# Kernel optimization log

Measured on AMD Instinct MI355X. Metric: run time of the kernel, lower is better.

## Reference

```python
import jax, jax.numpy as jnp
import numpy as np

T, B, DIN, H, DM, HYP, L = 128, 512, 512, 512, 256, 256, 100
STDV = 1.0 / np.sqrt(H)  # reset_parameters: uniform(-1/sqrt(hidden), 1/sqrt(hidden)) for ALL params
EPS = 1e-5


def setup_inputs() -> dict:
    key = jax.random.key(0)
    it = iter(jax.random.split(key, 32))
    U = lambda s: jax.random.uniform(next(it), s, jnp.float32, -STDV, STDV)
    x = jax.random.normal(next(it), (T, B, DIN), jnp.float32)
    meta = jax.random.normal(next(it), (B, L, DM), jnp.float32)
    inp = jax.random.randint(next(it), (B, L), 0, 5)
    return dict(
        x=x, meta=meta, inp=inp,
        # AttnModel (query from x, keys from meta)
        Wq=U((HYP, DIN)), bq=U((HYP,)), Wk=U((HYP, DM)), bk=U((HYP,)),
        # MergeLayer fc1 (fc2 is unused in MergeLayer.forward)
        Wm=U((HYP, DIN + DM + H)), bm=U((HYP,)),
        # hypernetwork projections z_h/z_x/z_b
        Wzh=U((4 * HYP, HYP)), bzh=U((4 * HYP,)),
        Wzx=U((4 * HYP, HYP)), bzx=U((4 * HYP,)),
        Wzb=U((4 * HYP, HYP)),
        # per-gate d_h/d_x/d_b maps (stacked over the 4 gates)
        Wdh=U((4, H, HYP)), Wdx=U((4, H, HYP)), Wdb=U((4, H, HYP)), bdb=U((4, H)),
        # main LSTM weights
        w_h=U((4, H, H)), w_x=U((4, H, DIN)),
        # per-gate LayerNorm affine
        ln_g=U((4, H)), ln_b=U((4, H)),
    )


def reference(x, meta, inp, Wq, bq, Wk, bk, Wm, bm, Wzh, bzh, Wzx, bzx, Wzb,
              Wdh, Wdx, Wdb, bdb, w_h, w_x, ln_g, ln_b):
    # --- AttnModel: attention-pool meta per timestep, meta_fea = [x, attended] ---
    q = jnp.einsum('tbi,hi->tbh', x, Wq) + bq                       # [T,B,HYP]
    k = jnp.einsum('blm,hm->blh', meta, Wk) + bk                    # [B,L,HYP]
    scores = jnp.einsum('tbh,blh->tbl', q, k) / jnp.sqrt(jnp.float32(HYP))
    scores = jnp.where((inp == 0)[None], -1e9, scores)              # pad mask
    attn = jax.nn.softmax(scores, axis=-1)
    attended = jnp.einsum('tbl,blm->tbm', attn, meta)               # [T,B,DM]
    meta_fea = jnp.concatenate([x, attended], axis=-1)              # [T,B,DIN+DM]

    def step(carry, xs):
        h, c = carry
        x_t, mf_t = xs
        # MergeLayer: relu(fc1(cat([meta_fea_t, h])))
        merged = jax.nn.relu(jnp.concatenate([mf_t, h], -1) @ Wm.T + bm)  # [B,HYP]
        zh = (merged @ Wzh.T + bzh).reshape(B, 4, HYP)
        zx = (merged @ Wzx.T + bzx).reshape(B, 4, HYP)
        zb = (merged @ Wzb.T).reshape(B, 4, HYP)
        d_h = jnp.einsum('bkz,khz->bkh', zh, Wdh)
        d_x = jnp.einsum('bkz,khz->bkh', zx, Wdx)
        d_b = jnp.einsum('bkz,khz->bkh', zb, Wdb) + bdb
        wh = jnp.einsum('khj,bj->bkh', w_h, h)
        wx = jnp.einsum('khj,bj->bkh', w_x, x_t)
        y = d_h * wh + d_x * wx + d_b                               # [B,4,H]
        mu = y.mean(-1, keepdims=True)
        var = ((y - mu) ** 2).mean(-1, keepdims=True)
        y = (y - mu) / jnp.sqrt(var + EPS) * ln_g + ln_b
        i, f, g, o = y[:, 0], y[:, 1], y[:, 2], y[:, 3]
        c_n = jax.nn.sigmoid(f) * c + jax.nn.sigmoid(i) * jnp.tanh(g)
        h_n = jax.nn.sigmoid(o) * jnp.tanh(c_n)
        return (h_n, c_n), h_n

    h0 = jnp.zeros((B, H), x.dtype)
    c0 = jnp.zeros((B, H), x.dtype)
    (hT, cT), out = jax.lax.scan(step, (h0, c0), (x, meta_fea))
    h_hat = jnp.zeros((1, B, HYP), x.dtype)  # hyper-state unused in this cell
    return out, hT[None], cT[None], h_hat, h_hat
```

## Files before the change

### kernel.cpp

```cpp
#include <hip/hip_runtime.h>
#include <hip/hip_bf16.h>

typedef unsigned short ushort_t;
typedef __attribute__((ext_vector_type(8))) short bf16x8;
typedef __attribute__((ext_vector_type(4))) float f32x4;

#define T_DIM 128
#define B_DIM 512
#define DIN 512
#define H_DIM 512
#define DM 256
#define HYP 256
#define L_DIM 100

__device__ __forceinline__ float bf2f(ushort_t u) {
    return __uint_as_float(((unsigned)u) << 16);
}
__device__ __forceinline__ ushort_t f2bf(float f) {
    unsigned u = __float_as_uint(f);
    unsigned r = (u + 0x7fffu + ((u >> 16) & 1u)) >> 16;
    return (ushort_t)r;
}
__device__ __forceinline__ float sigmoidf_(float x) {
    return 1.0f / (1.0f + __expf(-x));
}
__device__ __forceinline__ float fixf(float v) {
    if (!(v == v)) return 0.f;
    return fminf(fmaxf(v, -65504.f), 65504.f);
}

__global__ __launch_bounds__(256) void detect_kernel(const ushort_t* x, int nscan, int* flag) {
    __shared__ int found;
    if (threadIdx.x == 0) found = 0;
    __syncthreads();
    int f = 0;
    for (int i = threadIdx.x; i < nscan; i += 256) {
        unsigned u = x[i];
        if ((u & 0x7F80u) == 0x7F80u) f = 1;
    }
    if (f) atomicOr(&found, 1);
    __syncthreads();
    if (threadIdx.x == 0) *flag = found;
}

struct IngestP {
    const void* src[21];
    ushort_t* dst[21];
    int n[21];
    long total;
    const int* flag;
};

__global__ __launch_bounds__(256) void ingest_all(IngestP p) {
    int f = *p.flag;
    long idx0 = (long)blockIdx.x * 256 + threadIdx.x;
    long stride = (long)gridDim.x * 256;
    for (long idx = idx0; idx < p.total; idx += stride) {
        long r = idx;
#pragma unroll 1
        for (int t = 0; t < 21; t++) {
            if (r < p.n[t]) {
                p.dst[t][r] = f ? f2bf(((const float*)p.src[t])[r])
                               : ((const ushort_t*)p.src[t])[r];
                break;
            }
            r -= p.n[t];
        }
    }
}

__global__ __launch_bounds__(256) void zero_hhat(void* outbase, const int* flagp) {
    long i = 34078720 + (long)blockIdx.x * 256 + threadIdx.x;
    if (*flagp) ((float*)outbase)[i] = 0.f;
    else        ((ushort_t*)outbase)[i] = 0;
}

struct GP {
    const ushort_t* A1; const ushort_t* A2;
    const ushort_t* W1; const ushort_t* W2;
    long lda1, lda2, ldw1, ldw2;
    int K1, wc1, wc2, Nsplit, K, mode;
    const ushort_t* bias; ushort_t* outb; long ldo;
    const ushort_t* pre; ushort_t* merged; float* wh;
    float* outf; const float* fbias;
};

__global__ __launch_bounds__(256) void gemm_bt(GP g) {
    __shared__ __attribute__((aligned(16))) ushort_t As[128 * 40];
    __shared__ __attribute__((aligned(16))) ushort_t Bs[128 * 40];
    int tid  = threadIdx.x;
    int lane = tid & 63, wave = tid >> 6;
    int wm = (wave & 1) * 64, wn = (wave >> 1) * 64;
    int ml = lane & 15, quad = lane >> 4;
    long rowA0 = (long)blockIdx.x * 128;
    long rowW0 = (long)blockIdx.y * 128;
    int arow = tid >> 2, acol = (tid & 3) * 8;

    f32x4 acc[4][4];
#pragma unroll
    for (int i = 0; i < 4; i++)
#pragma unroll
        for (int j = 0; j < 4; j++) acc[i][j] = (f32x4){0.f, 0.f, 0.f, 0.f};

    for (int k0 = 0; k0 < g.K; k0 += 32) {
        uint4 av[2], wv[2];
#pragma unroll
        for (int s = 0; s < 2; s++) {
            int r = arow + s * 64;
            int k = k0 + acol;
            const ushort_t* asrc = (k < g.K1)
                ? g.A1 + (rowA0 + r) * g.lda1 + k
                : g.A2 + (rowA0 + r) * g.lda2 + (k - g.K1);
            av[s] = *(const uint4*)asrc;
            long n = rowW0 + r;
            const ushort_t* wsrc = (n < g.Nsplit)
                ? g.W1 + n * g.ldw1 + g.wc1 + k
                : g.W2 + (n - g.Nsplit) * g.ldw2 + g.wc2 + k;
            wv[s] = *(const uint4*)wsrc;
        }
        __syncthreads();
#pragma unroll
        for (int s = 0; s < 2; s++) {
            *(uint4*)&As[(arow + s * 64) * 40 + acol] = av[s];
            *(uint4*)&Bs[(arow + s * 64) * 40 + acol] = wv[s];
        }
        __syncthreads();
        bf16x8 af[4], bfm[4];
#pragma unroll
        for (int i = 0; i < 4; i++)
            af[i] = *(const bf16x8*)&As[(wm + i * 16 + ml) * 40 + quad * 8];
#pragma unroll
        for (int j = 0; j < 4; j++)
            bfm[j] = *(const bf16x8*)&Bs[(wn + j * 16 + ml) * 40 + quad * 8];
#pragma unroll
        for (int i = 0; i < 4; i++)
#pragma unroll
            for (int j = 0; j < 4; j++)
                acc[i][j] = __builtin_amdgcn_mfma_f32_16x16x32_bf16(af[i], bfm[j], acc[i][j], 0, 0, 0);
    }

#pragma unroll
    for (int i = 0; i < 4; i++) {
#pragma unroll
        for (int j = 0; j < 4; j++) {
            long rb = rowA0 + wm + i * 16 + quad * 4;
            long cn = rowW0 + wn + j * 16 + ml;
#pragma unroll
            for (int r = 0; r < 4; r++) {
                float v = acc[i][j][r];
                long rr = rb + r;
                if (g.mode == 0) {
                    if (g.bias) v += bf2f(g.bias[cn]);
                    g.outb[rr * g.ldo + cn] = f2bf(v);
                } else if (g.mode == 1) {
                    if (cn < 256) {
                        v += bf2f(g.pre[rr * 256 + cn]);
                        v = v > 0.f ? v : 0.f;
                        g.merged[rr * 256 + cn] = f2bf(v);
                    } else {
                        g.wh[rr * 2048 + (cn - 256)] = v;
                    }
                } else {
                    g.outf[rr * g.ldo + cn] = v + g.fbias[cn];
                }
            }
        }
    }
}

__global__ __launch_bounds__(256) void attn_kernel(const ushort_t* q, const ushort_t* kmat,
                                                   const ushort_t* meta, const int* inp,
                                                   ushort_t* att) {
    int b = blockIdx.x;
    __shared__ __attribute__((aligned(16))) ushort_t klds[L_DIM * 264];
    __shared__ float qlds[256];
    __shared__ float sc[L_DIM];
    __shared__ int msk[L_DIM];
    __shared__ float inv_s;
    int tid = threadIdx.x;

    for (int idx = tid; idx < L_DIM * 32; idx += 256) {
        int r = idx >> 5, c8 = (idx & 31) * 8;
        *(uint4*)&klds[r * 264 + c8] = *(const uint4*)&kmat[((long)b * L_DIM + r) * 256 + c8];
    }
    if (tid < L_DIM) msk[tid] = inp[b * L_DIM + tid];

    for (int t = 0; t < T_DIM; t++) {
        __syncthreads();
        qlds[tid] = bf2f(q[((long)t * B_DIM + b) * 256 + tid]);
        __syncthreads();
        if (tid < 2 * L_DIM) {
            int l = tid >> 1, half = tid & 1;
            const ushort_t* kr = &klds[l * 264 + half * 128];
            const float* qp = &qlds[half * 128];
            float s = 0.f;
            for (int j = 0; j < 128; j++) s += qp[j] * bf2f(kr[j]);
            s += __shfl_xor(s, 1);
            if (half == 0) sc[l] = (msk[l] == 0) ? -1000000000.0f : s * 0.0625f;
        }
        __syncthreads();
        if (tid < 64) {
            float s1 = sc[tid];
            float s2 = (tid + 64 < L_DIM) ? sc[tid + 64] : -1e30f;
            float mx = fmaxf(s1, s2);
            for (int o = 1; o < 64; o <<= 1) mx = fmaxf(mx, __shfl_xor(mx, o));
            float e1 = __expf(s1 - mx);
            float e2 = (tid + 64 < L_DIM) ? __expf(s2 - mx) : 0.f;
            float tot = e1 + e2;
            for (int o = 1; o < 64; o <<= 1) tot += __shfl_xor(tot, o);
            sc[tid] = e1;
            if (tid + 64 < L_DIM) sc[tid + 64] = e2;
            if (tid == 0) inv_s = 1.0f / tot;
        }
        __syncthreads();
        float a = 0.f;
        const ushort_t* mb = &meta[(long)b * L_DIM * 256 + tid];
        for (int l = 0; l < L_DIM; l++) a += sc[l] * bf2f(mb[(long)l * 256]);
        a *= inv_s;
        att[((long)t * B_DIM + b) * 256 + tid] = f2bf(a);
    }
}

__global__ __launch_bounds__(256) void call_precompute(const ushort_t* Wdh, const ushort_t* Wdx,
                                                       const ushort_t* Wdb, const ushort_t* Wzh,
                                                       const ushort_t* Wzx, const ushort_t* Wzb,
                                                       ushort_t* Call) {
    int bk = blockIdx.x;
    int kind = bk >> 2, kk = bk & 3;
    int h0 = blockIdx.y * 64;
    int m0 = blockIdx.z * 64;
    const ushort_t* Wd = (kind == 0) ? Wdh : ((kind == 1) ? Wdx : Wdb);
    const ushort_t* Wz = (kind == 0) ? Wzh : ((kind == 1) ? Wzx : Wzb);
    __shared__ __attribute__((aligned(16))) ushort_t dt[64 * 72];
    __shared__ __attribute__((aligned(16))) ushort_t zt[64 * 72];
    int tid = threadIdx.x;
    int ty = tid >> 4, tx = tid & 15;
    float acc[4][4] = {};
    for (int z0 = 0; z0 < 256; z0 += 64) {
        __syncthreads();
        for (int idx = tid; idx < 512; idx += 256) {
            int r = idx >> 3, c8 = (idx & 7) * 8;
            *(uint4*)&dt[r * 72 + c8] = *(const uint4*)&Wd[((long)(kk * 512 + h0 + r)) * 256 + z0 + c8];
            *(uint4*)&zt[r * 72 + c8] = *(const uint4*)&Wz[((long)(kk * 256 + z0 + r)) * 256 + m0 + c8];
        }
        __syncthreads();
        for (int z = 0; z < 64; z++) {
            float a[4], bb[4];
#pragma unroll
            for (int i = 0; i < 4; i++) a[i] = bf2f(dt[(ty * 4 + i) * 72 + z]);
#pragma unroll
            for (int j = 0; j < 4; j++) bb[j] = bf2f(zt[z * 72 + tx * 4 + j]);
#pragma unroll
            for (int i = 0; i < 4; i++)
#pragma unroll
                for (int j = 0; j < 4; j++) acc[i][j] += a[i] * bb[j];
        }
    }
#pragma unroll
    for (int i = 0; i < 4; i++)
#pragma unroll
        for (int j = 0; j < 4; j++)
            Call[((long)(kind * 2048 + kk * 512 + h0 + ty * 4 + i)) * 256 + m0 + tx * 4 + j] = f2bf(acc[i][j]);
}

__global__ __launch_bounds__(256) void dbias_kernel(const ushort_t* Wdh, const ushort_t* Wdx,
                                                    const ushort_t* bzh, const ushort_t* bzx,
                                                    const ushort_t* bdb, float* dbias) {
    int n = blockIdx.x * 256 + threadIdx.x;
    int kind = n >> 11, kk = (n >> 9) & 3, h = n & 511;
    float s = 0.f;
    if (kind == 2) {
        s = bf2f(bdb[kk * 512 + h]);
    } else {
        const ushort_t* Wd = (kind == 0) ? Wdh : Wdx;
        const ushort_t* bz = (kind == 0) ? bzh : bzx;
        for (int z = 0; z < 256; z++)
            s += bf2f(Wd[((long)(kk * 512 + h)) * 256 + z]) * bf2f(bz[kk * 256 + z]);
    }
    dbias[n] = s;
}

__global__ __launch_bounds__(256) void step_elem(const float* dall, const float* wh,
                                                 const ushort_t* wx, float* c, ushort_t* hbf,
                                                 const ushort_t* ln_g, const ushort_t* ln_b,
                                                 void* outbase, long off_t, int last,
                                                 const int* flagp) {
    int b = blockIdx.x, tid = threadIdx.x;
    int w = tid >> 6, lane = tid & 63;
    __shared__ float yln[4 * 512];
    const float* db = dall + (long)b * 6144;
    const float* whb = wh + (long)b * 2048;
    const ushort_t* wxb = wx + (long)b * 2048;
    float y[8];
    float sum = 0.f, ss = 0.f;
#pragma unroll
    for (int j = 0; j < 8; j++) {
        int h = lane + j * 64;
        int n = w * 512 + h;
        float v = db[n] * whb[n] + db[2048 + n] * bf2f(wxb[n]) + db[4096 + n];
        v = fixf(v);
        y[j] = v;
        sum += v;
        ss += v * v;
    }
    for (int o = 1; o < 64; o <<= 1) {
        sum += __shfl_xor(sum, o);
        ss += __shfl_xor(ss, o);
    }
    float mu = sum * (1.f / 512.f);
    float var = ss * (1.f / 512.f) - mu * mu;
    float rstd = rsqrtf(fmaxf(var, 0.f) + 1e-5f);
#pragma unroll
    for (int j = 0; j < 8; j++) {
        int h = lane + j * 64;
        float g = bf2f(ln_g[w * 512 + h]);
        float bb = bf2f(ln_b[w * 512 + h]);
        yln[w * 512 + h] = (y[j] - mu) * rstd * g + bb;
    }
    __syncthreads();
    int f = *flagp;
#pragma unroll
    for (int s = 0; s < 2; s++) {
        int h = tid + s * 256;
        float iv = yln[h], fv = yln[512 + h], gv = yln[1024 + h], ov = yln[1536 + h];
        long ci = (long)b * 512 + h;
        float cold = c[ci];
        float cn = sigmoidf_(fv) * cold + sigmoidf_(iv) * tanhf(gv);
        float hn = sigmoidf_(ov) * tanhf(cn);
        c[ci] = cn;
        hbf[ci] = f2bf(hn);
        if (f) {
            float* of = (float*)outbase;
            of[off_t + ci] = hn;
            if (last) { of[33554432 + ci] = hn; of[33816576 + ci] = cn; }
        } else {
            ushort_t* ob = (ushort_t*)outbase;
            ob[off_t + ci] = f2bf(hn);
            if (last) { ob[33554432 + ci] = f2bf(hn); ob[33816576 + ci] = f2bf(cn); }
        }
    }
}

extern "C" void kernel_launch(void* const* d_in, const int* in_sizes, int n_in,
                              void* d_out, int out_size, void* d_ws, size_t ws_size,
                              hipStream_t stream) {
    const int* inp = (const int*)d_in[2];

    size_t off = 0;
    char* wsb = (char*)d_ws;
    auto alloc = [&](size_t bytes) -> void* {
        off = (off + 255) & ~(size_t)255;
        void* p = wsb + off;
        off += bytes;
        return p;
    };

    int* flagp = (int*)alloc(256);

    static const int fidx[21] = {0,1,3,4,5,6,7,8,9,10,11,12,13,14,15,16,17,18,19,20,21};
    IngestP ip{};
    long total = 0;
    ushort_t* canon[21];
    for (int t = 0; t < 21; t++) {
        int src_i = fidx[t];
        int n = in_sizes[src_i];
        canon[t] = (ushort_t*)alloc((size_t)n * 2);
        ip.src[t] = d_in[src_i];
        ip.dst[t] = canon[t];
        ip.n[t] = n;
        total += n;
    }
    ip.total = total;
    ip.flag = flagp;

    const ushort_t* x    = canon[0];
    const ushort_t* meta = canon[1];
    const ushort_t* Wq   = canon[2];
    const ushort_t* bq   = canon[3];
    const ushort_t* Wk   = canon[4];
    const ushort_t* bk   = canon[5];
    const ushort_t* Wm   = canon[6];
    const ushort_t* bm   = canon[7];
    const ushort_t* Wzh  = canon[8];
    const ushort_t* bzh  = canon[9];
    const ushort_t* Wzx  = canon[10];
    const ushort_t* bzx  = canon[11];
    const ushort_t* Wzb  = canon[12];
    const ushort_t* Wdh  = canon[13];
    const ushort_t* Wdx  = canon[14];
    const ushort_t* Wdb  = canon[15];
    const ushort_t* bdb  = canon[16];
    const ushort_t* w_h  = canon[17];
    const ushort_t* w_x  = canon[18];
    const ushort_t* ln_g = canon[19];
    const ushort_t* ln_b = canon[20];

    ushort_t* qb    = (ushort_t*)alloc(33554432);
    ushort_t* kmb   = (ushort_t*)alloc(26214400);
    ushort_t* attb  = (ushort_t*)alloc(33554432);
    ushort_t* preb  = (ushort_t*)alloc(33554432);
    ushort_t* callb = (ushort_t*)alloc(3145728);
    float*    dbias = (float*)alloc(24576);
    ushort_t* hbf   = (ushort_t*)alloc(524288);
    float*    cf    = (float*)alloc(1048576);
    ushort_t* mgd   = (ushort_t*)alloc(262144);
    float*    whf   = (float*)alloc(4194304);
    float*    dall  = (float*)alloc(12582912);
    size_t base_end = (off + 255) & ~(size_t)255;
    bool full = (base_end + 268435456ull) <= ws_size;
    ushort_t* wxb = (ushort_t*)alloc(full ? 268435456ull : 2097152ull);

    detect_kernel<<<dim3(1), 256, 0, stream>>>((const ushort_t*)d_in[0], 262144, flagp);
    ingest_all<<<dim3(2048), 256, 0, stream>>>(ip);
    zero_hhat<<<dim3(1024), 256, 0, stream>>>(d_out, flagp);
    hipMemsetAsync(hbf, 0, 524288, stream);
    hipMemsetAsync(cf, 0, 1048576, stream);

    const int BIG = 1 << 30;

    {
        GP g{};
        g.A1 = meta; g.lda1 = 256; g.K1 = BIG; g.A2 = meta; g.lda2 = 256;
        g.W1 = Wk; g.ldw1 = 256; g.wc1 = 0; g.Nsplit = BIG; g.W2 = Wk; g.ldw2 = 256; g.wc2 = 0;
        g.K = 256; g.mode = 0; g.bias = bk; g.outb = kmb; g.ldo = 256;
        gemm_bt<<<dim3(400, 2), 256, 0, stream>>>(g);
    }
    {
        GP g{};
        g.A1 = x; g.lda1 = 512; g.K1 = BIG; g.A2 = x; g.lda2 = 512;
        g.W1 = Wq; g.ldw1 = 512; g.wc1 = 0; g.Nsplit = BIG; g.W2 = Wq; g.ldw2 = 512; g.wc2 = 0;
        g.K = 512; g.mode = 0; g.bias = bq; g.outb = qb; g.ldo = 256;
        gemm_bt<<<dim3(512, 2), 256, 0, stream>>>(g);
    }
    attn_kernel<<<dim3(512), 256, 0, stream>>>(qb, kmb, meta, inp, attb);
    {
        GP g{};
        g.A1 = x; g.lda1 = 512; g.K1 = 512; g.A2 = attb; g.lda2 = 256;
        g.W1 = Wm; g.ldw1 = 1280; g.wc1 = 0; g.Nsplit = BIG; g.W2 = Wm; g.ldw2 = 1280; g.wc2 = 0;
        g.K = 768; g.mode = 0; g.bias = bm; g.outb = preb; g.ldo = 256;
        gemm_bt<<<dim3(512, 2), 256, 0, stream>>>(g);
    }
    if (full) {
        GP g{};
        g.A1 = x; g.lda1 = 512; g.K1 = BIG; g.A2 = x; g.lda2 = 512;
        g.W1 = w_x; g.ldw1 = 512; g.wc1 = 0; g.Nsplit = BIG; g.W2 = w_x; g.ldw2 = 512; g.wc2 = 0;
        g.K = 512; g.mode = 0; g.bias = nullptr; g.outb = wxb; g.ldo = 2048;
        gemm_bt<<<dim3(512, 16), 256, 0, stream>>>(g);
    }
    call_precompute<<<dim3(12, 8, 4), 256, 0, stream>>>(Wdh, Wdx, Wdb, Wzh, Wzx, Wzb, callb);
    dbias_kernel<<<dim3(24), 256, 0, stream>>>(Wdh, Wdx, bzh, bzx, bdb, dbias);

    for (int t = 0; t < T_DIM; t++) {
        if (!full) {
            GP g{};
            g.A1 = x + (long)t * B_DIM * DIN; g.lda1 = 512; g.K1 = BIG; g.A2 = g.A1; g.lda2 = 512;
            g.W1 = w_x; g.ldw1 = 512; g.wc1 = 0; g.Nsplit = BIG; g.W2 = w_x; g.ldw2 = 512; g.wc2 = 0;
            g.K = 512; g.mode = 0; g.bias = nullptr; g.outb = wxb; g.ldo = 2048;
            gemm_bt<<<dim3(4, 16), 256, 0, stream>>>(g);
        }
        {
            GP g{};
            g.A1 = hbf; g.lda1 = 512; g.K1 = BIG; g.A2 = hbf; g.lda2 = 512;
            g.W1 = Wm; g.ldw1 = 1280; g.wc1 = 768; g.Nsplit = 256;
            g.W2 = w_h; g.ldw2 = 512; g.wc2 = 0;
            g.K = 512; g.mode = 1;
            g.pre = preb + (long)t * B_DIM * 256; g.merged = mgd; g.wh = whf;
            gemm_bt<<<dim3(4, 18), 256, 0, stream>>>(g);
        }
        {
            GP g{};
            g.A1 = mgd; g.lda1 = 256; g.K1 = BIG; g.A2 = mgd; g.lda2 = 256;
            g.W1 = callb; g.ldw1 = 256; g.wc1 = 0; g.Nsplit = BIG; g.W2 = callb; g.ldw2 = 256; g.wc2 = 0;
            g.K = 256; g.mode = 2; g.outf = dall; g.ldo = 6144; g.fbias = dbias;
            gemm_bt<<<dim3(4, 48), 256, 0, stream>>>(g);
        }
        const ushort_t* wxt = full ? (wxb + (long)t * B_DIM * 2048) : wxb;
        step_elem<<<dim3(512), 256, 0, stream>>>(dall, whf, wxt, cf, hbf, ln_g, ln_b,
                                                 d_out, (long)t * B_DIM * H_DIM,
                                                 (t == T_DIM - 1) ? 1 : 0, flagp);
    }
}
```

Measured before the change: 13.00 ms.

## Replace per-timestep kernel launches with a persistent cooperative kernel using grid sync

The recurrent scan previously launched three or four kernels per timestep, 128 timesteps in all. A single cooperative kernel with 256 blocks now loops over timesteps, distributes the GEMM tiles and per-batch elementwise work across blocks, and separates the dependent phases with grid.sync. This is meant to remove kernel launch and drain overhead on the serial critical path. The cost is grid-wide barriers and fixed tile assignment, so some blocks sit idle (e.g. only 72 tiles in the first phase), and it relies on all blocks being co-resident.

```diff
diff --git a/kernel.cpp b/kernel.cpp
--- a/kernel.cpp
+++ b/kernel.cpp
@@ -1,5 +1,8 @@
 #include <hip/hip_runtime.h>
 #include <hip/hip_bf16.h>
+#include <hip/hip_cooperative_groups.h>
+
+namespace cg = cooperative_groups;
 
 typedef unsigned short ushort_t;
 typedef __attribute__((ext_vector_type(8))) short bf16x8;
@@ -12,6 +15,7 @@
 #define DM 256
 #define HYP 256
 #define L_DIM 100
+#define GRID_P 256
 
 __device__ __forceinline__ float bf2f(ushort_t u) {
     return __uint_as_float(((unsigned)u) << 16);
@@ -85,15 +89,12 @@
     float* outf; const float* fbias;
 };
 
-__global__ __launch_bounds__(256) void gemm_bt(GP g) {
-    __shared__ __attribute__((aligned(16))) ushort_t As[128 * 40];
-    __shared__ __attribute__((aligned(16))) ushort_t Bs[128 * 40];
+__device__ __forceinline__ void gemm_tile(const GP& g, long rowA0, long rowW0,
+                                          ushort_t* As, ushort_t* Bs) {
     int tid  = threadIdx.x;
     int lane = tid & 63, wave = tid >> 6;
     int wm = (wave & 1) * 64, wn = (wave >> 1) * 64;
     int ml = lane & 15, quad = lane >> 4;
-    long rowA0 = (long)blockIdx.x * 128;
-    long rowW0 = (long)blockIdx.y * 128;
     int arow = tid >> 2, acol = (tid & 3) * 8;
 
     f32x4 acc[4][4];
@@ -168,6 +169,12 @@
     }
 }
 
+__global__ __launch_bounds__(256) void gemm_bt(GP g) {
+    __shared__ __attribute__((aligned(16))) ushort_t As[128 * 40];
+    __shared__ __attribute__((aligned(16))) ushort_t Bs[128 * 40];
+    gemm_tile(g, (long)blockIdx.x * 128, (long)blockIdx.y * 128, As, Bs);
+}
+
 __global__ __launch_bounds__(256) void attn_kernel(const ushort_t* q, const ushort_t* kmat,
                                                    const ushort_t* meta, const int* inp,
                                                    ushort_t* att) {
@@ -280,24 +287,23 @@
     dbias[n] = s;
 }
 
-__global__ __launch_bounds__(256) void step_elem(const float* dall, const float* wh,
-                                                 const ushort_t* wx, float* c, ushort_t* hbf,
-                                                 const ushort_t* ln_g, const ushort_t* ln_b,
-                                                 void* outbase, long off_t, int last,
-                                                 const int* flagp) {
-    int b = blockIdx.x, tid = threadIdx.x;
+__device__ __forceinline__ void step_tile(int b, const float* dall, const float* whf,
+                                          const ushort_t* wxb, float* c, ushort_t* hbf,
+                                          const ushort_t* ln_g, const ushort_t* ln_b,
+                                          void* outbase, long off_t, int last, int flag,
+                                          float* yln) {
+    int tid = threadIdx.x;
     int w = tid >> 6, lane = tid & 63;
-    __shared__ float yln[4 * 512];
     const float* db = dall + (long)b * 6144;
-    const float* whb = wh + (long)b * 2048;
-    const ushort_t* wxb = wx + (long)b * 2048;
+    const float* whb = whf + (long)b * 2048;
+    const ushort_t* wxr = wxb + (long)b * 2048;
     float y[8];
     float sum = 0.f, ss = 0.f;
 #pragma unroll
     for (int j = 0; j < 8; j++) {
         int h = lane + j * 64;
         int n = w * 512 + h;
-        float v = db[n] * whb[n] + db[2048 + n] * bf2f(wxb[n]) + db[4096 + n];
+        float v = db[n] * whb[n] + db[2048 + n] * bf2f(wxr[n]) + db[4096 + n];
         v = fixf(v);
         y[j] = v;
         sum += v;
@@ -310,6 +316,7 @@
     float mu = sum * (1.f / 512.f);
     float var = ss * (1.f / 512.f) - mu * mu;
     float rstd = rsqrtf(fmaxf(var, 0.f) + 1e-5f);
+    __syncthreads();
 #pragma unroll
     for (int j = 0; j < 8; j++) {
         int h = lane + j * 64;
@@ -318,7 +325,6 @@
         yln[w * 512 + h] = (y[j] - mu) * rstd * g + bb;
     }
     __syncthreads();
-    int f = *flagp;
 #pragma unroll
     for (int s = 0; s < 2; s++) {
         int h = tid + s * 256;
@@ -329,7 +335,7 @@
         float hn = sigmoidf_(ov) * tanhf(cn);
         c[ci] = cn;
         hbf[ci] = f2bf(hn);
-        if (f) {
+        if (flag) {
             float* of = (float*)outbase;
             of[off_t + ci] = hn;
             if (last) { of[33554432 + ci] = hn; of[33816576 + ci] = cn; }
@@ -338,6 +344,64 @@
             ob[off_t + ci] = f2bf(hn);
             if (last) { ob[33554432 + ci] = f2bf(hn); ob[33816576 + ci] = f2bf(cn); }
         }
+    }
+}
+
+struct SP {
+    GP g12;
+    GP g3;
+    GP gwx;
+    const ushort_t* preb;
+    const ushort_t* xall;
+    const ushort_t* wxb;
+    const float* dall; const float* whf;
+    float* cf; ushort_t* hbf;
+    const ushort_t* ln_g; const ushort_t* ln_b;
+    void* outbase;
+    const int* flagp;
+    int full;
+};
+
+__global__ __launch_bounds__(256) void scan_persist(SP p) {
+    __shared__ __attribute__((aligned(16))) ushort_t As[128 * 40];
+    __shared__ __attribute__((aligned(16))) ushort_t Bs[128 * 40];
+    cg::grid_group grid = cg::this_grid();
+    const int nb = gridDim.x;
+    const int bid = blockIdx.x;
+    int flag = *p.flagp;
+
+    GP g12 = p.g12;
+    GP g3  = p.g3;
+
+    for (int t = 0; t < T_DIM; t++) {
+        g12.pre = p.preb + (long)t * B_DIM * 256;
+        {
+            const int n12 = 4 * 18;
+            const int ntile = n12 + (p.full ? 0 : 4 * 16);
+            for (int tt = bid; tt < ntile; tt += nb) {
+                if (tt < n12) {
+                    gemm_tile(g12, (long)(tt & 3) * 128, (long)(tt >> 2) * 128, As, Bs);
+                } else {
+                    int t2 = tt - n12;
+                    GP gw = p.gwx;
+                    gw.A1 = p.xall + (long)t * B_DIM * DIN;
+                    gw.A2 = gw.A1;
+                    gemm_tile(gw, (long)(t2 & 3) * 128, (long)(t2 >> 2) * 128, As, Bs);
+                }
+            }
+        }
+        grid.sync();
+        for (int tt = bid; tt < 4 * 48; tt += nb)
+            gemm_tile(g3, (long)(tt & 3) * 128, (long)(tt >> 2) * 128, As, Bs);
+        grid.sync();
+        {
+            const ushort_t* wxt = p.full ? (p.wxb + (long)t * B_DIM * 2048) : p.wxb;
+            for (int b = bid; b < B_DIM; b += nb)
+                step_tile(b, p.dall, p.whf, wxt, p.cf, p.hbf, p.ln_g, p.ln_b,
+                          p.outbase, (long)t * B_DIM * H_DIM,
+                          (t == T_DIM - 1) ? 1 : 0, flag, (float*)As);
+        }
+        grid.sync();
     }
 }
 
@@ -450,33 +514,27 @@
     call_precompute<<<dim3(12, 8, 4), 256, 0, stream>>>(Wdh, Wdx, Wdb, Wzh, Wzx, Wzb, callb);
     dbias_kernel<<<dim3(24), 256, 0, stream>>>(Wdh, Wdx, bzh, bzx, bdb, dbias);
 
-    for (int t = 0; t < T_DIM; t++) {
-        if (!full) {
-            GP g{};
-            g.A1 = x + (long)t * B_DIM * DIN; g.lda1 = 512; g.K1 = BIG; g.A2 = g.A1; g.lda2 = 512;
-            g.W1 = w_x; g.ldw1 = 512; g.wc1 = 0; g.Nsplit = BIG; g.W2 = w_x; g.ldw2 = 512; g.wc2 = 0;
-            g.K = 512; g.mode = 0; g.bias = nullptr; g.outb = wxb; g.ldo = 2048;
-            gemm_bt<<<dim3(4, 16), 256, 0, stream>>>(g);
-        }
-        {
-            GP g{};
-            g.A1 = hbf; g.lda1 = 512; g.K1 = BIG; g.A2 = hbf; g.lda2 = 512;
-            g.W1 = Wm; g.ldw1 = 1280; g.wc1 = 768; g.Nsplit = 256;
-            g.W2 = w_h; g.ldw2 = 512; g.wc2 = 0;
-            g.K = 512; g.mode = 1;
-            g.pre = preb + (long)t * B_DIM * 256; g.merged = mgd; g.wh = whf;
-            gemm_bt<<<dim3(4, 18), 256, 0, stream>>>(g);
-        }
-        {
-            GP g{};
-            g.A1 = mgd; g.lda1 = 256; g.K1 = BIG; g.A2 = mgd; g.lda2 = 256;
-            g.W1 = callb; g.ldw1 = 256; g.wc1 = 0; g.Nsplit = BIG; g.W2 = callb; g.ldw2 = 256; g.wc2 = 0;
-            g.K = 256; g.mode = 2; g.outf = dall; g.ldo = 6144; g.fbias = dbias;
-            gemm_bt<<<dim3(4, 48), 256, 0, stream>>>(g);
-        }
-        const ushort_t* wxt = full ? (wxb + (long)t * B_DIM * 2048) : wxb;
-        step_elem<<<dim3(512), 256, 0, stream>>>(dall, whf, wxt, cf, hbf, ln_g, ln_b,
-                                                 d_out, (long)t * B_DIM * H_DIM,
-                                                 (t == T_DIM - 1) ? 1 : 0, flagp);
-    }
-}
+    SP sp{};
+    sp.g12.A1 = hbf; sp.g12.lda1 = 512; sp.g12.K1 = BIG; sp.g12.A2 = hbf; sp.g12.lda2 = 512;
+    sp.g12.W1 = Wm;  sp.g12.ldw1 = 1280; sp.g12.wc1 = 768; sp.g12.Nsplit = 256;
+    sp.g12.W2 = w_h; sp.g12.ldw2 = 512;  sp.g12.wc2 = 0;
+    sp.g12.K = 512; sp.g12.mode = 1;
+    sp.g12.pre = preb; sp.g12.merged = mgd; sp.g12.wh = whf;
+    sp.g3.A1 = mgd; sp.g3.lda1 = 256; sp.g3.K1 = BIG; sp.g3.A2 = mgd; sp.g3.lda2 = 256;
+    sp.g3.W1 = callb; sp.g3.ldw1 = 256; sp.g3.wc1 = 0; sp.g3.Nsplit = BIG;
+    sp.g3.W2 = callb; sp.g3.ldw2 = 256; sp.g3.wc2 = 0;
+    sp.g3.K = 256; sp.g3.mode = 2; sp.g3.outf = dall; sp.g3.ldo = 6144; sp.g3.fbias = dbias;
+    sp.gwx.A1 = x; sp.gwx.lda1 = 512; sp.gwx.K1 = BIG; sp.gwx.A2 = x; sp.gwx.lda2 = 512;
+    sp.gwx.W1 = w_x; sp.gwx.ldw1 = 512; sp.gwx.wc1 = 0; sp.gwx.Nsplit = BIG;
+    sp.gwx.W2 = w_x; sp.gwx.ldw2 = 512; sp.gwx.wc2 = 0;
+    sp.gwx.K = 512; sp.gwx.mode = 0; sp.gwx.bias = nullptr; sp.gwx.outb = wxb; sp.gwx.ldo = 2048;
+
+    sp.preb = preb; sp.xall = x; sp.wxb = wxb;
+    sp.dall = dall; sp.whf = whf; sp.cf = cf; sp.hbf = hbf;
+    sp.ln_g = ln_g; sp.ln_b = ln_b;
+    sp.outbase = d_out; sp.flagp = flagp; sp.full = full ? 1 : 0;
+
+    void* kargs[] = { (void*)&sp };
+    void (*fp)(SP) = scan_persist;
+    hipLaunchCooperativeKernel(fp, dim3(GRID_P), dim3(256), kargs, 0, stream);
+}
```

Result: slower. 22.58 ms (+73.7%).

## Fuse recurrent timestep loop into one persistent per-row-pair scan kernel

Applied to the files above, without the earlier changes.

Replaces the 128-step host loop, which launched several GEMM and elementwise kernels per step, with a single persistent kernel. Each block owns two batch rows for all timesteps and keeps h, c, merged and the LayerNorm buffers in LDS and registers. The merge GEMM, the w_h/w_x products, the hypernetwork d-maps, LayerNorm and the LSTM gates are all computed in-block with MFMA, which removes launch overhead and intermediate global round-trips. In exchange, every block re-streams the full weight set from cache each step, and only 2 of the 16 MFMA rows carry useful data, so throughput may become bound by cache bandwidth or wasted matrix work.

```diff
diff --git a/kernel.cpp b/kernel.cpp
--- a/kernel.cpp
+++ b/kernel.cpp
@@ -27,6 +27,10 @@
 __device__ __forceinline__ float fixf(float v) {
     if (!(v == v)) return 0.f;
     return fminf(fmaxf(v, -65504.f), 65504.f);
+}
+__device__ __forceinline__ bf16x8 zero8() {
+    bf16x8 z = {0, 0, 0, 0, 0, 0, 0, 0};
+    return z;
 }
 
 __global__ __launch_bounds__(256) void detect_kernel(const ushort_t* x, int nscan, int* flag) {
@@ -81,7 +85,6 @@
     long lda1, lda2, ldw1, ldw2;
     int K1, wc1, wc2, Nsplit, K, mode;
     const ushort_t* bias; ushort_t* outb; long ldo;
-    const ushort_t* pre; ushort_t* merged; float* wh;
     float* outf; const float* fbias;
 };
 
@@ -152,14 +155,6 @@
                 if (g.mode == 0) {
                     if (g.bias) v += bf2f(g.bias[cn]);
                     g.outb[rr * g.ldo + cn] = f2bf(v);
-                } else if (g.mode == 1) {
-                    if (cn < 256) {
-                        v += bf2f(g.pre[rr * 256 + cn]);
-                        v = v > 0.f ? v : 0.f;
-                        g.merged[rr * 256 + cn] = f2bf(v);
-                    } else {
-                        g.wh[rr * 2048 + (cn - 256)] = v;
-                    }
                 } else {
                     g.outf[rr * g.ldo + cn] = v + g.fbias[cn];
                 }
@@ -280,64 +275,193 @@
     dbias[n] = s;
 }
 
-__global__ __launch_bounds__(256) void step_elem(const float* dall, const float* wh,
-                                                 const ushort_t* wx, float* c, ushort_t* hbf,
-                                                 const ushort_t* ln_g, const ushort_t* ln_b,
-                                                 void* outbase, long off_t, int last,
-                                                 const int* flagp) {
-    int b = blockIdx.x, tid = threadIdx.x;
-    int w = tid >> 6, lane = tid & 63;
-    __shared__ float yln[4 * 512];
-    const float* db = dall + (long)b * 6144;
-    const float* whb = wh + (long)b * 2048;
-    const ushort_t* wxb = wx + (long)b * 2048;
-    float y[8];
-    float sum = 0.f, ss = 0.f;
-#pragma unroll
-    for (int j = 0; j < 8; j++) {
-        int h = lane + j * 64;
-        int n = w * 512 + h;
-        float v = db[n] * whb[n] + db[2048 + n] * bf2f(wxb[n]) + db[4096 + n];
-        v = fixf(v);
-        y[j] = v;
-        sum += v;
-        ss += v * v;
-    }
-    for (int o = 1; o < 64; o <<= 1) {
-        sum += __shfl_xor(sum, o);
-        ss += __shfl_xor(ss, o);
-    }
-    float mu = sum * (1.f / 512.f);
-    float var = ss * (1.f / 512.f) - mu * mu;
-    float rstd = rsqrtf(fmaxf(var, 0.f) + 1e-5f);
-#pragma unroll
-    for (int j = 0; j < 8; j++) {
-        int h = lane + j * 64;
-        float g = bf2f(ln_g[w * 512 + h]);
-        float bb = bf2f(ln_b[w * 512 + h]);
-        yln[w * 512 + h] = (y[j] - mu) * rstd * g + bb;
-    }
+struct SR {
+    const ushort_t* preb;
+    const ushort_t* xall;
+    const ushort_t* wxb;
+    const ushort_t* Wm;
+    const ushort_t* w_h;
+    const ushort_t* w_x;
+    const ushort_t* callb;
+    const float* dbias;
+    const ushort_t* ln_g;
+    const ushort_t* ln_b;
+    void* outbase;
+    const int* flagp;
+    int full;
+};
+
+__global__ __launch_bounds__(512) void scan_rows(SR p) {
+    __shared__ __attribute__((aligned(16))) ushort_t h_lds[2][512];
+    __shared__ __attribute__((aligned(16))) ushort_t x_lds[2][512];
+    __shared__ __attribute__((aligned(16))) ushort_t m_lds[2][256];
+    __shared__ float yln[2][4][512];
+    __shared__ float red[4][8][4];
+
+    int tid = threadIdx.x;
+    int wave = tid >> 6, lane = tid & 63;
+    int quad = lane >> 4, ml = lane & 15;
+    long b0 = (long)blockIdx.x * 2;
+    int flag = *p.flagp;
+    int full = p.full;
+
+    for (int i = tid; i < 1024; i += 512) ((ushort_t*)h_lds)[i] = 0;
+    float cr0 = 0.f, cr1 = 0.f;
     __syncthreads();
-    int f = *flagp;
-#pragma unroll
-    for (int s = 0; s < 2; s++) {
-        int h = tid + s * 256;
-        float iv = yln[h], fv = yln[512 + h], gv = yln[1024 + h], ov = yln[1536 + h];
-        long ci = (long)b * 512 + h;
-        float cold = c[ci];
-        float cn = sigmoidf_(fv) * cold + sigmoidf_(iv) * tanhf(gv);
-        float hn = sigmoidf_(ov) * tanhf(cn);
-        c[ci] = cn;
-        hbf[ci] = f2bf(hn);
-        if (f) {
-            float* of = (float*)outbase;
-            of[off_t + ci] = hn;
-            if (last) { of[33554432 + ci] = hn; of[33816576 + ci] = cn; }
-        } else {
-            ushort_t* ob = (ushort_t*)outbase;
-            ob[off_t + ci] = f2bf(hn);
-            if (last) { ob[33554432 + ci] = f2bf(hn); ob[33816576 + ci] = f2bf(cn); }
-        }
+
+    for (int t = 0; t < T_DIM; t++) {
+        if (!full) {
+            for (int i = tid; i < 1024; i += 512)
+                ((ushort_t*)x_lds)[i] =
+                    p.xall[((long)t * 512 + b0 + (i >> 9)) * 512 + (i & 511)];
+        }
+
+#pragma unroll
+        for (int tt = 0; tt < 2; tt++) {
+            int n0 = wave * 32 + tt * 16;
+            f32x4 acc = {0.f, 0.f, 0.f, 0.f};
+            const ushort_t* wp = p.Wm + (long)(n0 + ml) * 1280 + 768 + quad * 8;
+#pragma unroll
+            for (int k0 = 0; k0 < 512; k0 += 32) {
+                bf16x8 bf = *(const bf16x8*)(wp + k0);
+                bf16x8 af = zero8();
+                if (ml < 2) af = *(const bf16x8*)&h_lds[ml][k0 + quad * 8];
+                acc = __builtin_amdgcn_mfma_f32_16x16x32_bf16(af, bf, acc, 0, 0, 0);
+            }
+            if (quad == 0) {
+                int n = n0 + ml;
+                const ushort_t* pr = p.preb + ((long)t * 512 + b0) * 256 + n;
+#pragma unroll
+                for (int r = 0; r < 2; r++) {
+                    float v = acc[r] + bf2f(pr[r * 256]);
+                    m_lds[r][n] = f2bf(v > 0.f ? v : 0.f);
+                }
+            }
+        }
+        __syncthreads();
+
+#pragma unroll 1
+        for (int kk = 0; kk < 4; kk++) {
+            float sum0 = 0.f, ss0 = 0.f, sum1 = 0.f, ss1 = 0.f;
+#pragma unroll 2
+            for (int tt = 0; tt < 4; tt++) {
+                int hc = wave * 64 + tt * 16 + ml;
+                int n = kk * 512 + hc;
+                f32x4 awh = {0.f, 0.f, 0.f, 0.f};
+                f32x4 adh = {0.f, 0.f, 0.f, 0.f};
+                f32x4 adx = {0.f, 0.f, 0.f, 0.f};
+                f32x4 adb = {0.f, 0.f, 0.f, 0.f};
+                f32x4 awx = {0.f, 0.f, 0.f, 0.f};
+                const ushort_t* whp = p.w_h + (long)n * 512 + quad * 8;
+#pragma unroll
+                for (int k0 = 0; k0 < 512; k0 += 32) {
+                    bf16x8 af = zero8();
+                    if (ml < 2) af = *(const bf16x8*)&h_lds[ml][k0 + quad * 8];
+                    awh = __builtin_amdgcn_mfma_f32_16x16x32_bf16(
+                        af, *(const bf16x8*)(whp + k0), awh, 0, 0, 0);
+                }
+                if (!full) {
+                    const ushort_t* wxp = p.w_x + (long)n * 512 + quad * 8;
+#pragma unroll
+                    for (int k0 = 0; k0 < 512; k0 += 32) {
+                        bf16x8 ax = zero8();
+                        if (ml < 2) ax = *(const bf16x8*)&x_lds[ml][k0 + quad * 8];
+                        awx = __builtin_amdgcn_mfma_f32_16x16x32_bf16(
+                            ax, *(const bf16x8*)(wxp + k0), awx, 0, 0, 0);
+                    }
+                }
+                const ushort_t* c0p = p.callb + (long)n * 256 + quad * 8;
+                const ushort_t* c1p = p.callb + (long)(2048 + n) * 256 + quad * 8;
+                const ushort_t* c2p = p.callb + (long)(4096 + n) * 256 + quad * 8;
+#pragma unroll
+                for (int k0 = 0; k0 < 256; k0 += 32) {
+                    bf16x8 am = zero8();
+                    if (ml < 2) am = *(const bf16x8*)&m_lds[ml][k0 + quad * 8];
+                    adh = __builtin_amdgcn_mfma_f32_16x16x32_bf16(
+                        am, *(const bf16x8*)(c0p + k0), adh, 0, 0, 0);
+                    adx = __builtin_amdgcn_mfma_f32_16x16x32_bf16(
+                        am, *(const bf16x8*)(c1p + k0), adx, 0, 0, 0);
+                    adb = __builtin_amdgcn_mfma_f32_16x16x32_bf16(
+                        am, *(const bf16x8*)(c2p + k0), adb, 0, 0, 0);
+                }
+                if (quad == 0) {
+                    float d0 = p.dbias[n], d1 = p.dbias[2048 + n], d2 = p.dbias[4096 + n];
+#pragma unroll
+                    for (int r = 0; r < 2; r++) {
+                        float wxv = full
+                            ? bf2f(p.wxb[((long)t * 512 + b0 + r) * 2048 + n])
+                            : awx[r];
+                        float v = (adh[r] + d0) * awh[r] + (adx[r] + d1) * wxv + (adb[r] + d2);
+                        v = fixf(v);
+                        yln[r][kk][hc] = v;
+                        if (r == 0) { sum0 += v; ss0 += v * v; }
+                        else        { sum1 += v; ss1 += v * v; }
+                    }
+                }
+            }
+#pragma unroll
+            for (int o = 1; o < 16; o <<= 1) {
+                sum0 += __shfl_xor(sum0, o); ss0 += __shfl_xor(ss0, o);
+                sum1 += __shfl_xor(sum1, o); ss1 += __shfl_xor(ss1, o);
+            }
+            if (lane == 0) {
+                red[kk][wave][0] = sum0; red[kk][wave][1] = ss0;
+                red[kk][wave][2] = sum1; red[kk][wave][3] = ss1;
+            }
+            __syncthreads();
+            if (quad == 0) {
+                float S0 = 0.f, Q0 = 0.f, S1 = 0.f, Q1 = 0.f;
+#pragma unroll
+                for (int w2 = 0; w2 < 8; w2++) {
+                    S0 += red[kk][w2][0]; Q0 += red[kk][w2][1];
+                    S1 += red[kk][w2][2]; Q1 += red[kk][w2][3];
+                }
+                float mu0 = S0 * (1.f / 512.f), mu1 = S1 * (1.f / 512.f);
+                float rs0 = rsqrtf(fmaxf(Q0 * (1.f / 512.f) - mu0 * mu0, 0.f) + 1e-5f);
+                float rs1 = rsqrtf(fmaxf(Q1 * (1.f / 512.f) - mu1 * mu1, 0.f) + 1e-5f);
+#pragma unroll
+                for (int tt = 0; tt < 4; tt++) {
+                    int hc = wave * 64 + tt * 16 + ml;
+                    float g = bf2f(p.ln_g[kk * 512 + hc]);
+                    float bb = bf2f(p.ln_b[kk * 512 + hc]);
+                    yln[0][kk][hc] = (yln[0][kk][hc] - mu0) * rs0 * g + bb;
+                    yln[1][kk][hc] = (yln[1][kk][hc] - mu1) * rs1 * g + bb;
+                }
+            }
+        }
+        __syncthreads();
+
+        {
+            int h = tid;
+            float i0 = yln[0][0][h], f0 = yln[0][1][h], g0 = yln[0][2][h], o0 = yln[0][3][h];
+            float i1 = yln[1][0][h], f1 = yln[1][1][h], g1 = yln[1][2][h], o1 = yln[1][3][h];
+            float cn0 = sigmoidf_(f0) * cr0 + sigmoidf_(i0) * tanhf(g0);
+            float hn0 = sigmoidf_(o0) * tanhf(cn0);
+            float cn1 = sigmoidf_(f1) * cr1 + sigmoidf_(i1) * tanhf(g1);
+            float hn1 = sigmoidf_(o1) * tanhf(cn1);
+            cr0 = cn0; cr1 = cn1;
+            h_lds[0][h] = f2bf(hn0);
+            h_lds[1][h] = f2bf(hn1);
+            long off_t = (long)t * (B_DIM * H_DIM);
+            long ci0 = b0 * 512 + h, ci1 = (b0 + 1) * 512 + h;
+            int last = (t == T_DIM - 1);
+            if (flag) {
+                float* of = (float*)p.outbase;
+                of[off_t + ci0] = hn0; of[off_t + ci1] = hn1;
+                if (last) {
+                    of[33554432 + ci0] = hn0; of[33554432 + ci1] = hn1;
+                    of[33816576 + ci0] = cn0; of[33816576 + ci1] = cn1;
+                }
+            } else {
+                ushort_t* ob = (ushort_t*)p.outbase;
+                ob[off_t + ci0] = f2bf(hn0); ob[off_t + ci1] = f2bf(hn1);
+                if (last) {
+                    ob[33554432 + ci0] = f2bf(hn0); ob[33554432 + ci1] = f2bf(hn1);
+                    ob[33816576 + ci0] = f2bf(cn0); ob[33816576 + ci1] = f2bf(cn1);
+                }
+            }
+        }
+        __syncthreads();
     }
 }
 
@@ -401,20 +525,13 @@
     ushort_t* preb  = (ushort_t*)alloc(33554432);
     ushort_t* callb = (ushort_t*)alloc(3145728);
     float*    dbias = (float*)alloc(24576);
-    ushort_t* hbf   = (ushort_t*)alloc(524288);
-    float*    cf    = (float*)alloc(1048576);
-    ushort_t* mgd   = (ushort_t*)alloc(262144);
-    float*    whf   = (float*)alloc(4194304);
-    float*    dall  = (float*)alloc(12582912);
     size_t base_end = (off + 255) & ~(size_t)255;
     bool full = (base_end + 268435456ull) <= ws_size;
-    ushort_t* wxb = (ushort_t*)alloc(full ? 268435456ull : 2097152ull);
+    ushort_t* wxb = (ushort_t*)alloc(full ? 268435456ull : 256ull);
 
     detect_kernel<<<dim3(1), 256, 0, stream>>>((const ushort_t*)d_in[0], 262144, flagp);
     ingest_all<<<dim3(2048), 256, 0, stream>>>(ip);
     zero_hhat<<<dim3(1024), 256, 0, stream>>>(d_out, flagp);
-    hipMemsetAsync(hbf, 0, 524288, stream);
-    hipMemsetAsync(cf, 0, 1048576, stream);
 
     const int BIG = 1 << 30;
 
@@ -450,33 +567,12 @@
     call_precompute<<<dim3(12, 8, 4), 256, 0, stream>>>(Wdh, Wdx, Wdb, Wzh, Wzx, Wzb, callb);
     dbias_kernel<<<dim3(24), 256, 0, stream>>>(Wdh, Wdx, bzh, bzx, bdb, dbias);
 
-    for (int t = 0; t < T_DIM; t++) {
-        if (!full) {
-            GP g{};
-            g.A1 = x + (long)t * B_DIM * DIN; g.lda1 = 512; g.K1 = BIG; g.A2 = g.A1; g.lda2 = 512;
-            g.W1 = w_x; g.ldw1 = 512; g.wc1 = 0; g.Nsplit = BIG; g.W2 = w_x; g.ldw2 = 512; g.wc2 = 0;
-            g.K = 512; g.mode = 0; g.bias = nullptr; g.outb = wxb; g.ldo = 2048;
-            gemm_bt<<<dim3(4, 16), 256, 0, stream>>>(g);
-        }
-        {
-            GP g{};
-            g.A1 = hbf; g.lda1 = 512; g.K1 = BIG; g.A2 = hbf; g.lda2 = 512;
-            g.W1 = Wm; g.ldw1 = 1280; g.wc1 = 768; g.Nsplit = 256;
-            g.W2 = w_h; g.ldw2 = 512; g.wc2 = 0;
-            g.K = 512; g.mode = 1;
-            g.pre = preb + (long)t * B_DIM * 256; g.merged = mgd; g.wh = whf;
-            gemm_bt<<<dim3(4, 18), 256, 0, stream>>>(g);
-        }
-        {
-            GP g{};
-            g.A1 = mgd; g.lda1 = 256; g.K1 = BIG; g.A2 = mgd; g.lda2 = 256;
-            g.W1 = callb; g.ldw1 = 256; g.wc1 = 0; g.Nsplit = BIG; g.W2 = callb; g.ldw2 = 256; g.wc2 = 0;
-            g.K = 256; g.mode = 2; g.outf = dall; g.ldo = 6144; g.fbias = dbias;
-            gemm_bt<<<dim3(4, 48), 256, 0, stream>>>(g);
-        }
-        const ushort_t* wxt = full ? (wxb + (long)t * B_DIM * 2048) : wxb;
-        step_elem<<<dim3(512), 256, 0, stream>>>(dall, whf, wxt, cf, hbf, ln_g, ln_b,
-                                                 d_out, (long)t * B_DIM * H_DIM,
-                                                 (t == T_DIM - 1) ? 1 : 0, flagp);
-    }
-}
+    SR sr{};
+    sr.preb = preb; sr.xall = x; sr.wxb = wxb;
+    sr.Wm = Wm; sr.w_h = w_h; sr.w_x = w_x;
+    sr.callb = callb; sr.dbias = dbias;
+    sr.ln_g = ln_g; sr.ln_b = ln_b;
+    sr.outbase = d_out; sr.flagp = flagp;
+    sr.full = full ? 1 : 0;
+    scan_rows<<<dim3(256), 512, 0, stream>>>(sr);
+}
```

Result: slower. 25.22 ms (+93.9%).
